# Kernel tuning notes

Measured on AMD Instinct MI355X. Metric: run time of the kernel, lower is better.

Reference implementation:

```python
import jax, jax.numpy as jnp
import numpy as np

# Mamba3/SSD selective state-space mixer (scalar-A-per-head SSD recurrence,
# causal depthwise conv on x/B/C, gated RMSNorm, in/out projections).
D_MODEL = 1024
EXPAND = 2
D_INNER = EXPAND * D_MODEL            # 2048
HEADDIM = D_MODEL // 16               # 64  (head_count=16 -> headdim 64)
NHEADS = D_INNER // HEADDIM           # 32
D_STATE = 128
CONV_W = 4
CONV_DIM = D_INNER + 2 * D_STATE      # x, B, C share the conv
D_IN_PROJ = 2 * D_INNER + 2 * D_STATE + NHEADS  # z, x, B, C, dt
EPS = 1e-5


def setup_inputs() -> dict:
    key = jax.random.key(0)
    ks = jax.random.split(key, 8)
    B, L = 4, 2048
    hidden = jax.random.normal(ks[0], (B, L, D_MODEL), dtype=jnp.float32)
    W_in = jax.random.normal(ks[1], (D_MODEL, D_IN_PROJ), dtype=jnp.float32) * 0.02
    conv_w = jax.random.normal(ks[2], (CONV_DIM, CONV_W), dtype=jnp.float32) * 0.2
    conv_b = jnp.zeros((CONV_DIM,), dtype=jnp.float32)
    # dt_bias: inverse-softplus of dt ~ U[1e-3, 0.1]
    dt = jnp.exp(jax.random.uniform(ks[3], (NHEADS,)) * (np.log(0.1) - np.log(1e-3)) + np.log(1e-3))
    dt_bias = dt + jnp.log(-jnp.expm1(-dt))
    A_log = jnp.log(jax.random.uniform(ks[4], (NHEADS,), minval=1.0, maxval=16.0))
    D = jnp.ones((NHEADS,), dtype=jnp.float32)
    norm_w = jnp.ones((D_INNER,), dtype=jnp.float32)
    W_out = jax.random.normal(ks[5], (D_INNER, D_MODEL), dtype=jnp.float32) * 0.02
    return {"hidden": hidden, "W_in": W_in, "conv_w": conv_w, "conv_b": conv_b,
            "dt_bias": dt_bias, "A_log": A_log, "D": D, "norm_w": norm_w, "W_out": W_out}


def _silu(x):
    return x * jax.nn.sigmoid(x)


def _mixer(hidden, W_in, conv_w, conv_b, dt_bias, A_log, D, norm_w, W_out):
    Bsz, L, _ = hidden.shape
    zxbcdt = hidden @ W_in                                    # [B,L,D_IN_PROJ]
    z = zxbcdt[..., :D_INNER]
    xBC = zxbcdt[..., D_INNER:D_INNER + CONV_DIM]
    dt = zxbcdt[..., -NHEADS:]                                # [B,L,H]
    # causal depthwise conv, width 4 (small fixed loop over taps)
    xp = jnp.pad(xBC, ((0, 0), (CONV_W - 1, 0), (0, 0)))
    conv = sum(xp[:, k:k + L, :] * conv_w[:, k] for k in range(CONV_W))
    xBC = _silu(conv + conv_b)
    x = xBC[..., :D_INNER].reshape(Bsz, L, NHEADS, HEADDIM)   # [B,L,H,P]
    Bm = xBC[..., D_INNER:D_INNER + D_STATE]                  # [B,L,N]
    Cm = xBC[..., D_INNER + D_STATE:]                         # [B,L,N]
    dt = jax.nn.softplus(dt + dt_bias)                        # [B,L,H]
    dA = jnp.exp(dt * (-jnp.exp(A_log)))                      # [B,L,H] decay in (0,1)
    dBx = jnp.einsum('blh,bln,blhp->blhpn', dt, Bm, x)        # [B,L,H,P,N]

    def step(h, inp):
        dA_t, dBx_t, C_t = inp                                # [B,H],[B,H,P,N],[B,N]
        h = dA_t[:, :, None, None] * h + dBx_t
        y = jnp.einsum('bhpn,bn->bhp', h, C_t)
        return h, y

    h0 = jnp.zeros((Bsz, NHEADS, HEADDIM, D_STATE), dtype=hidden.dtype)
    xs = (jnp.moveaxis(dA, 1, 0), jnp.moveaxis(dBx, 1, 0), jnp.moveaxis(Cm, 1, 0))
    _, ys = jax.lax.scan(step, h0, xs)                        # [L,B,H,P]
    y = jnp.moveaxis(ys, 0, 1) + D[None, None, :, None] * x   # skip term
    y = y.reshape(Bsz, L, D_INNER)
    # gated RMSNorm: norm(y * silu(z))
    y = y * _silu(z)
    y = y * jax.lax.rsqrt(jnp.mean(y * y, axis=-1, keepdims=True) + EPS) * norm_w
    return y @ W_out


def reference(hidden, W_in, conv_w, conv_b, dt_bias, A_log, D, norm_w, W_out):
    return _mixer(hidden, W_in, conv_w, conv_b, dt_bias, A_log, D, norm_w, W_out)
```

## Files before the change

kernel.cpp:

```cpp
#include <hip/hip_runtime.h>
#include <math.h>

#define BSZ 4
#define LEN 2048
#define DM 1024
#define DI 2048
#define HD 64
#define NH 32
#define DS 128
#define CD 2304
#define DP 4384
#define NTOK (BSZ*LEN)
#define QCH 128
#define NCH (LEN/QCH)
#define TOFF (DP-NH)

#define CONV_R 64
#define NRB (NTOK/CONV_R)
#define NPAD 4352

typedef unsigned short ushort_t;
typedef __bf16 bf16x8 __attribute__((ext_vector_type(8)));
typedef ushort_t us8 __attribute__((ext_vector_type(8)));
typedef float f32x4 __attribute__((ext_vector_type(4)));

__device__ __forceinline__ ushort_t f2bf(float f) {
    unsigned u = __float_as_uint(f);
    unsigned r = (u + 0x7FFFu + ((u >> 16) & 1u)) >> 16;
    return (ushort_t)r;
}
__device__ __forceinline__ float bf2f(ushort_t u) {
    return __uint_as_float(((unsigned)u) << 16);
}
__device__ __forceinline__ bf16x8 us2bf(us8 v) {
    union { us8 u; bf16x8 b; } x; x.u = v; return x.b;
}

__device__ __forceinline__ void gl_lds16(const void* g, void* l) {
    __builtin_amdgcn_global_load_lds(
        (const __attribute__((address_space(1))) void*)g,
        (__attribute__((address_space(3))) void*)l, 16, 0, 0);
}

__global__ __launch_bounds__(256) void cvt_bf16(
    const float* __restrict__ A, ushort_t* __restrict__ Ab)
{
    size_t i = ((size_t)blockIdx.x * 256 + threadIdx.x) * 4;
    float4 v = *(const float4*)(A + i);
    ushort_t o[4] = { f2bf(v.x), f2bf(v.y), f2bf(v.z), f2bf(v.w) };
    *(uint2*)(Ab + i) = *(uint2*)o;
}

__global__ __launch_bounds__(256) void transpose_cvt(
    const float* __restrict__ W, ushort_t* __restrict__ Wt,
    const float* __restrict__ colscale, int K, int N, int ldw)
{
    __shared__ float T[32][33];
    const int n0 = blockIdx.x * 32;
    const int k0 = blockIdx.y * 32;
    const int tid = threadIdx.x;
    #pragma unroll
    for (int l = 0; l < 4; l++) {
        int idx = tid + l * 256;
        int ki = idx >> 5, nj = idx & 31;
        int n = n0 + nj;
        float s = colscale ? colscale[k0 + ki] : 1.f;
        T[ki][nj] = (n < N) ? W[(size_t)(k0 + ki) * ldw + n] * s : 0.f;
    }
    __syncthreads();
    #pragma unroll
    for (int l = 0; l < 4; l++) {
        int idx = tid + l * 256;
        int nj = idx >> 5, ki = idx & 31;
        Wt[(size_t)(n0 + nj) * K + k0 + ki] = f2bf(T[ki][nj]);
    }
}

__global__ __launch_bounds__(256, 3) void gemm1_tb(
    const ushort_t* __restrict__ A, const ushort_t* __restrict__ Bt,
    ushort_t* __restrict__ C, int K, int lda, int ldb, int ldc)
{
    __shared__ __align__(16) ushort_t LA[3][128 * 32];
    __shared__ __align__(16) ushort_t LB[3][128 * 32];
    const int tid = threadIdx.x;
    int bid = blockIdx.y * gridDim.x + blockIdx.x;
    const int nwg = gridDim.x * gridDim.y;
    if (!(nwg & 7)) bid = (bid & 7) * (nwg >> 3) + (bid >> 3);
    const int n0 = (bid % gridDim.x) * 128;
    const int m0 = (bid / gridDim.x) * 128;
    const int lane = tid & 63;
    const int w = tid >> 6;
    const int wm = w >> 1, wn = w & 1;
    const int lm = lane & 15, quad = lane >> 4;
    const int ck = ((quad * 16) ^ (((lm >> 1) & 3) << 4)) >> 1;

    const int srow = tid >> 2;
    const int scolb = ((tid & 3) * 16) ^ (((tid >> 3) & 3) << 4);
    const char* gA = (const char*)A + ((size_t)(m0 + srow) * lda) * 2 + scolb;
    const char* gB = (const char*)Bt + ((size_t)(n0 + srow) * ldb) * 2 + scolb;
    const size_t strA = (size_t)64 * lda * 2;
    const size_t strB = (size_t)64 * ldb * 2;
    const int ldst = tid * 8;

    f32x4 acc[4][4];
    #pragma unroll
    for (int i = 0; i < 4; i++)
        #pragma unroll
        for (int j = 0; j < 4; j++) acc[i][j] = (f32x4){0.f, 0.f, 0.f, 0.f};

    const int NTt = K >> 5;

    auto STAGE = [&](int kt1, int buf) {
        const char* a = gA + (size_t)kt1 * 64;
        const char* b = gB + (size_t)kt1 * 64;
        gl_lds16(a + 0 * strA, &LA[buf][0 * 2048 + ldst]);
        gl_lds16(a + 1 * strA, &LA[buf][1 * 2048 + ldst]);
        gl_lds16(b + 0 * strB, &LB[buf][0 * 2048 + ldst]);
        gl_lds16(b + 1 * strB, &LB[buf][1 * 2048 + ldst]);
    };

    STAGE(0, 0);
    STAGE(1, 1);

    int cur = 0;
    int sb  = 2;
    for (int kt = 0; kt < NTt; ++kt) {
        __builtin_amdgcn_s_barrier();
        const int ahead = NTt - 1 - kt;
        if (ahead >= 2) {
            STAGE(kt + 2, sb);
            asm volatile("s_waitcnt vmcnt(8)" ::: "memory");
        } else if (ahead == 1) {
            asm volatile("s_waitcnt vmcnt(4)" ::: "memory");
        } else {
            asm volatile("s_waitcnt vmcnt(0)" ::: "memory");
        }
        __builtin_amdgcn_s_barrier();

        bf16x8 af[4], bf[4];
        #pragma unroll
        for (int s = 0; s < 4; s++)
            af[s] = *(const bf16x8*)&LA[cur][((wm * 64 + s * 16 + lm) << 5) + ck];
        #pragma unroll
        for (int t = 0; t < 4; t++)
            bf[t] = *(const bf16x8*)&LB[cur][((wn * 64 + t * 16 + lm) << 5) + ck];
        __builtin_amdgcn_s_setprio(1);
        #pragma unroll
        for (int s = 0; s < 4; s++)
            #pragma unroll
            for (int t = 0; t < 4; t++)
                acc[s][t] = __builtin_amdgcn_mfma_f32_16x16x32_bf16(
                    af[s], bf[t], acc[s][t], 0, 0, 0);
        __builtin_amdgcn_s_setprio(0);

        cur = (cur == 2) ? 0 : cur + 1;
        sb  = (sb == 2) ? 0 : sb + 1;
    }

    #pragma unroll
    for (int s = 0; s < 4; s++) {
        const int row = m0 + wm * 64 + s * 16 + quad * 4;
        #pragma unroll
        for (int t = 0; t < 4; t++) {
            const int col = n0 + wn * 64 + t * 16 + lm;
            #pragma unroll
            for (int r = 0; r < 4; r++)
                C[(size_t)(row + r) * ldc + col] = f2bf(acc[s][t][r]);
        }
    }
}

template <bool OB>
__global__ __launch_bounds__(256) void gemm128(
    const ushort_t* __restrict__ A, const ushort_t* __restrict__ Bt,
    void* __restrict__ Cp, const float* __restrict__ rowscale,
    int K, int lda, int ldb, int ldc)
{
    __shared__ __align__(16) ushort_t LA[2][128 * 64];
    __shared__ __align__(16) ushort_t LB[2][128 * 64];
    const int tid = threadIdx.x;
    int bid = blockIdx.y * gridDim.x + blockIdx.x;
    const int nwg = gridDim.x * gridDim.y;
    if (!(nwg & 7)) bid = (bid & 7) * (nwg >> 3) + (bid >> 3);
    const int n0 = (bid % gridDim.x) * 128;
    const int m0 = (bid / gridDim.x) * 128;
    const int lane = tid & 63;
    const int w = tid >> 6;
    const int wm = w >> 1, wn = w & 1;
    const int lm = lane & 15, quad = lane >> 4;
    const int swz = (lm & 7) << 4;
    const int ck0 = ((0 * 64 + quad * 16) ^ swz) >> 1;
    const int ck1 = ((1 * 64 + quad * 16) ^ swz) >> 1;

    const int srow = tid >> 3;
    const int scolb = ((tid & 7) * 16) ^ ((srow & 7) << 4);
    const char* gA = (const char*)A + ((size_t)(m0 + srow) * lda) * 2 + scolb;
    const char* gB = (const char*)Bt + ((size_t)(n0 + srow) * ldb) * 2 + scolb;
    const size_t strA = (size_t)32 * lda * 2;
    const size_t strB = (size_t)32 * ldb * 2;
    const int ldst = tid * 8;

    f32x4 acc[4][4];
    #pragma unroll
    for (int i = 0; i < 4; i++)
        #pragma unroll
        for (int j = 0; j < 4; j++) acc[i][j] = (f32x4){0.f, 0.f, 0.f, 0.f};

    const int NTt = K >> 6;

    auto STAGE = [&](int kt1, int nxt) {
        const char* a = gA + (size_t)kt1 * 128;
        const char* b = gB + (size_t)kt1 * 128;
        #pragma unroll
        for (int j = 0; j < 4; j++)
            gl_lds16(a + j * strA, &LA[nxt][j * 2048 + ldst]);
        #pragma unroll
        for (int j = 0; j < 4; j++)
            gl_lds16(b + j * strB, &LB[nxt][j * 2048 + ldst]);
    };

    STAGE(0, 0);

    for (int kt = 0; kt < NTt; ++kt) {
        const int cur = kt & 1;
        __builtin_amdgcn_s_barrier();
        if (kt + 1 < NTt) {
            STAGE(kt + 1, cur ^ 1);
            asm volatile("s_waitcnt vmcnt(8)" ::: "memory");
        } else {
            asm volatile("s_waitcnt vmcnt(0)" ::: "memory");
        }
        __builtin_amdgcn_s_barrier();

        bf16x8 af[4][2], bf[4][2];
        #pragma unroll
        for (int s = 0; s < 4; s++) {
            const int rb = (wm * 64 + s * 16 + lm) << 6;
            af[s][0] = *(const bf16x8*)&LA[cur][rb + ck0];
            af[s][1] = *(const bf16x8*)&LA[cur][rb + ck1];
        }
        #pragma unroll
        for (int t = 0; t < 4; t++) {
            const int rb = (wn * 64 + t * 16 + lm) << 6;
            bf[t][0] = *(const bf16x8*)&LB[cur][rb + ck0];
            bf[t][1] = *(const bf16x8*)&LB[cur][rb + ck1];
        }
        __builtin_amdgcn_s_setprio(1);
        #pragma unroll
        for (int kk = 0; kk < 2; kk++)
            #pragma unroll
            for (int s = 0; s < 4; s++)
                #pragma unroll
                for (int t = 0; t < 4; t++)
                    acc[s][t] = __builtin_amdgcn_mfma_f32_16x16x32_bf16(
                        af[s][kk], bf[t][kk], acc[s][t], 0, 0, 0);
        __builtin_amdgcn_s_setprio(0);
    }

    #pragma unroll
    for (int s = 0; s < 4; s++) {
        const int row = m0 + wm * 64 + s * 16 + quad * 4;
        float rs[4] = {1.f, 1.f, 1.f, 1.f};
        if (!OB && rowscale) {
            #pragma unroll
            for (int r = 0; r < 4; r++)
                rs[r] = rsqrtf(rowscale[row + r] * (1.f / DI) + 1e-5f);
        }
        #pragma unroll
        for (int t = 0; t < 4; t++) {
            const int col = n0 + wn * 64 + t * 16 + lm;
            #pragma unroll
            for (int r = 0; r < 4; r++) {
                if (OB)
                    ((ushort_t*)Cp)[(size_t)(row + r) * ldc + col] = f2bf(acc[s][t][r]);
                else
                    ((float*)Cp)[(size_t)(row + r) * ldc + col] = acc[s][t][r] * rs[r];
            }
        }
    }
}

__global__ __launch_bounds__(256) void conv_silu_bf16(
    const ushort_t* __restrict__ xbcb, const float* __restrict__ cw,
    const float* __restrict__ cb, ushort_t* __restrict__ xT,
    ushort_t* __restrict__ Bn, ushort_t* __restrict__ BT,
    ushort_t* __restrict__ Cn)
{
    __shared__ ushort_t Tl[256][68];
    const int tid = threadIdx.x;
    const int c = blockIdx.x * 256 + tid;
    const int rb = blockIdx.y;
    const int row0 = rb * CONV_R;
    const bool isBC = (blockIdx.x == 8);

    const float w0 = cw[c*4+0], w1 = cw[c*4+1], w2 = cw[c*4+2], w3 = cw[c*4+3];
    const float bias = cb[c];
    float h0 = 0.f, h1 = 0.f, h2 = 0.f;
    if ((row0 & (LEN - 1)) != 0) {
        h0 = bf2f(xbcb[(size_t)(row0 - 3) * NPAD + c]);
        h1 = bf2f(xbcb[(size_t)(row0 - 2) * NPAD + c]);
        h2 = bf2f(xbcb[(size_t)(row0 - 1) * NPAD + c]);
    }
    const ushort_t* p = xbcb + (size_t)row0 * NPAD + c;
    for (int r = 0; r < CONV_R; r++) {
        float xin = bf2f(*p);
        float a = bias + w0*h0 + w1*h1 + w2*h2 + w3*xin;
        ushort_t bv = f2bf(a / (1.f + __expf(-a)));
        Tl[tid][r] = bv;
        if (isBC) {
            int row = row0 + r;
            if (tid < DS) Bn[(size_t)row * DS + tid] = bv;
            else          Cn[(size_t)row * DS + (tid - DS)] = bv;
        }
        h0 = h1; h1 = h2; h2 = xin;
        p += NPAD;
    }
    __syncthreads();

    const int seg = tid & 7;
    const int clb = tid >> 3;
    if (!isBC) {
        #pragma unroll
        for (int pass = 0; pass < 8; pass++) {
            int cl = pass * 32 + clb;
            int cc = blockIdx.x * 256 + cl;
            us8 v;
            #pragma unroll
            for (int j = 0; j < 8; j++) v[j] = Tl[cl][seg * 8 + j];
            *(us8*)&xT[(size_t)cc * NTOK + row0 + seg * 8] = v;
        }
    } else {
        #pragma unroll
        for (int pass = 0; pass < 4; pass++) {
            int n = pass * 32 + clb;
            us8 v;
            #pragma unroll
            for (int j = 0; j < 8; j++) v[j] = Tl[n][seg * 8 + j];
            *(us8*)&BT[(size_t)n * NTOK + row0 + seg * 8] = v;
        }
    }
}

__global__ __launch_bounds__(256) void gct_gemm(
    const ushort_t* __restrict__ Bn, const ushort_t* __restrict__ Cn,
    float* __restrict__ Graw)
{
    const int bc = blockIdx.x;
    const int chunk = bc % NCH;
    const int b = bc / NCH;
    const size_t rowbase = (size_t)b * LEN + (size_t)chunk * QCH;
    const int tid = threadIdx.x;
    const int w = tid >> 6, lane = tid & 63;
    const int lm = lane & 15, quad = lane >> 4;
    const int tw0 = w * 32;

    f32x4 acc[2][8];
    #pragma unroll
    for (int ti = 0; ti < 2; ti++)
        #pragma unroll
        for (int sj = 0; sj < 8; sj++) acc[ti][sj] = (f32x4){0.f, 0.f, 0.f, 0.f};

    #pragma unroll
    for (int ks = 0; ks < 4; ks++) {
        const int k0 = ks * 32 + quad * 8;
        bf16x8 a0 = *(const bf16x8*)&Cn[(rowbase + tw0 + lm) * DS + k0];
        bf16x8 a1 = *(const bf16x8*)&Cn[(rowbase + tw0 + 16 + lm) * DS + k0];
        #pragma unroll
        for (int sj = 0; sj < 8; sj++) {
            bf16x8 bb = *(const bf16x8*)&Bn[(rowbase + sj * 16 + lm) * DS + k0];
            acc[0][sj] = __builtin_amdgcn_mfma_f32_16x16x32_bf16(a0, bb, acc[0][sj], 0, 0, 0);
            acc[1][sj] = __builtin_amdgcn_mfma_f32_16x16x32_bf16(a1, bb, acc[1][sj], 0, 0, 0);
        }
    }
    float* G = Graw + (size_t)bc * (QCH * QCH);
    #pragma unroll
    for (int ti = 0; ti < 2; ti++)
        #pragma unroll
        for (int sj = 0; sj < 8; sj++)
            #pragma unroll
            for (int r = 0; r < 4; r++)
                G[(size_t)(tw0 + ti * 16 + quad * 4 + r) * QCH + sj * 16 + lm] = acc[ti][sj][r];
}

__global__ __launch_bounds__(256) void dt_proc_fp32(
    const float* __restrict__ hidden, const float* __restrict__ W_in,
    const float* __restrict__ dt_bias, const float* __restrict__ A_log,
    float* __restrict__ dtv, float* __restrict__ ldA)
{
    const int h = threadIdx.x & 31;
    const int tt = threadIdx.x >> 5;
    const int t = blockIdx.x * 8 + tt;
    const float* hr = hidden + (size_t)t * DM;
    const float* wc = W_in + TOFF + h;
    float a0 = 0.f, a1 = 0.f, a2 = 0.f, a3 = 0.f;
    for (int k = 0; k < DM; k += 4) {
        a0 += hr[k+0] * wc[(size_t)(k+0) * DP];
        a1 += hr[k+1] * wc[(size_t)(k+1) * DP];
        a2 += hr[k+2] * wc[(size_t)(k+2) * DP];
        a3 += hr[k+3] * wc[(size_t)(k+3) * DP];
    }
    float v = (a0 + a1) + (a2 + a3) + dt_bias[h];
    float sp = (v > 20.f) ? v : log1pf(expf(v));
    int idx = t * NH + h;
    dtv[idx] = sp;
    ldA[idx] = -sp * expf(A_log[h]);
}

__global__ __launch_bounds__(64) void scan_chunk(
    const float* __restrict__ dtv, const float* __restrict__ ldA,
    float* __restrict__ lcpb, float* __restrict__ dtsb,
    float* __restrict__ coefb, float* __restrict__ csum)
{
    const int blk = blockIdx.x;
    const int chunk = blk % NCH;
    const int bh = blk / NCH;
    const int h = bh % NH;
    const int b = bh / NH;
    const int lane = threadIdx.x;
    const size_t rowbase = (size_t)b * LEN + (size_t)chunk * QCH;
    const int t0 = 2 * lane, t1 = 2 * lane + 1;
    float v0 = ldA[(rowbase + t0) * NH + h];
    float v1 = ldA[(rowbase + t1) * NH + h];
    float d0 = dtv[(rowbase + t0) * NH + h];
    float d1 = dtv[(rowbase + t1) * NH + h];
    float pair = v0 + v1;
    #pragma unroll
    for (int off = 1; off < 64; off <<= 1) {
        float n = __shfl_up(pair, off, 64);
        if (lane >= off) pair += n;
    }
    float l1 = pair, l0 = pair - v1;
    float total = __shfl(pair, 63, 64);
    size_t base = (size_t)blk * QCH;
    *(float2*)&lcpb[base + t0] = make_float2(l0, l1);
    *(float2*)&dtsb[base + t0] = make_float2(d0, d1);
    *(float2*)&coefb[base + t0] =
        make_float2(__expf(total - l0) * d0, __expf(total - l1) * d1);
    if (lane == 63) csum[blk] = total;
}

__global__ __launch_bounds__(256) void phase1_mfma(
    const ushort_t* __restrict__ xT, const ushort_t* __restrict__ BT,
    const float* __restrict__ coefb, float* __restrict__ S)
{
    const int h = blockIdx.x & (NH - 1);
    const int bc = blockIdx.x >> 5;
    const int chunk = bc % NCH;
    const int b = bc / NCH;
    const int blko = (b * NH + h) * NCH + chunk;
    const int tid = threadIdx.x;
    const size_t rowbase = (size_t)b * LEN + (size_t)chunk * QCH;

    __shared__ float coef[QCH];
    if (tid < QCH) coef[tid] = coefb[(size_t)blko * QCH + tid];
    __syncthreads();

    const int w = tid >> 6, lane = tid & 63;
    const int lm = lane & 15, quad = lane >> 4;
    const int nw0 = w * 32;

    f32x4 acc[4][2];
    #pragma unroll
    for (int i = 0; i < 4; i++)
        #pragma unroll
        for (int j = 0; j < 2; j++) acc[i][j] = (f32x4){0.f, 0.f, 0.f, 0.f};

    #pragma unroll
    for (int ks = 0; ks < 4; ks++) {
        const int k0 = ks * 32 + quad * 8;
        bf16x8 a[4];
        #pragma unroll
        for (int mi = 0; mi < 4; mi++)
            a[mi] = *(const bf16x8*)&xT[(size_t)(h * HD + mi * 16 + lm) * NTOK + rowbase + k0];
        float cf[8];
        #pragma unroll
        for (int j = 0; j < 8; j++) cf[j] = coef[k0 + j];
        #pragma unroll
        for (int ni = 0; ni < 2; ni++) {
            us8 raw = *(const us8*)&BT[(size_t)(nw0 + ni * 16 + lm) * NTOK + rowbase + k0];
            us8 sb;
            #pragma unroll
            for (int j = 0; j < 8; j++) sb[j] = f2bf(bf2f(raw[j]) * cf[j]);
            bf16x8 bfr = us2bf(sb);
            __builtin_amdgcn_s_setprio(1);
            #pragma unroll
            for (int mi = 0; mi < 4; mi++)
                acc[mi][ni] = __builtin_amdgcn_mfma_f32_16x16x32_bf16(a[mi], bfr, acc[mi][ni], 0, 0, 0);
            __builtin_amdgcn_s_setprio(0);
        }
    }
    float* Sb = S + (size_t)blko * (HD * DS);
    #pragma unroll
    for (int mi = 0; mi < 4; mi++)
        #pragma unroll
        for (int ni = 0; ni < 2; ni++)
            #pragma unroll
            for (int r = 0; r < 4; r++)
                Sb[(size_t)(mi * 16 + quad * 4 + r) * DS + nw0 + ni * 16 + lm] = acc[mi][ni][r];
}

__global__ __launch_bounds__(256) void phase2(
    const float* __restrict__ S, const float* __restrict__ csum,
    ushort_t* __restrict__ hsb)
{
    const int bh = blockIdx.x >> 3;
    const int esl = blockIdx.x & 7;
    const int tid = threadIdx.x;
    const int eb = esl * 1024 + tid;
    float run[4] = {0.f, 0.f, 0.f, 0.f};
    for (int c = 0; c < NCH; c++) {
        float P = __expf(csum[bh * NCH + c]);
        size_t base = (size_t)(bh * NCH + c) * (HD * DS);
        #pragma unroll
        for (int i = 0; i < 4; i++) {
            size_t idx = base + eb + i * 256;
            float s = S[idx];
            hsb[idx] = f2bf(run[i]);
            run[i] = P * run[i] + s;
        }
    }
}

__global__ __launch_bounds__(256) void phase3_mfma(
    const ushort_t* __restrict__ xT, const ushort_t* __restrict__ Cn,
    const ushort_t* __restrict__ hsb, const float* __restrict__ Graw,
    const float* __restrict__ lcpb, const float* __restrict__ dtsb,
    const float* __restrict__ Dvec, ushort_t* __restrict__ zxb,
    float* __restrict__ ss)
{
    const int tid = threadIdx.x;
    const int h = blockIdx.x & (NH - 1);
    const int bc = blockIdx.x >> 5;
    const int chunk = bc % NCH;
    const int b = bc / NCH;
    const int blko = (b * NH + h) * NCH + chunk;
    const size_t rowbase = (size_t)b * LEN + (size_t)chunk * QCH;

    __shared__ float lcp[QCH];
    __shared__ float dts[QCH];
    if (tid < QCH) {
        lcp[tid] = lcpb[(size_t)blko * QCH + tid];
        dts[tid] = dtsb[(size_t)blko * QCH + tid];
    }
    __syncthreads();

    const int w = tid >> 6, lane = tid & 63;
    const int lm = lane & 15, quad = lane >> 4;
    const int tw0 = w * 32;

    const float* Gr = Graw + (size_t)bc * (QCH * QCH);
    const ushort_t* hsp = hsb + (size_t)blko * (HD * DS);

    f32x4 acc2[2][4];
    #pragma unroll
    for (int ti = 0; ti < 2; ti++)
        #pragma unroll
        for (int pi = 0; pi < 4; pi++) acc2[ti][pi] = (f32x4){0.f, 0.f, 0.f, 0.f};

    #pragma unroll
    for (int ks = 0; ks < 8; ks++) {
        bf16x8 a[2], bb[4];
        if (ks < 4) {
            const int k0 = ks * 32 + quad * 8;
            #pragma unroll
            for (int ti = 0; ti < 2; ti++) {
                int t = tw0 + ti * 16 + lm;
                float lt = lcp[t];
                const float* gp = Gr + (size_t)t * QCH + k0;
                float4 g0 = *(const float4*)gp;
                float4 g1 = *(const float4*)(gp + 4);
                float ge[8] = { g0.x, g0.y, g0.z, g0.w, g1.x, g1.y, g1.z, g1.w };
                us8 sb;
                #pragma unroll
                for (int j = 0; j < 8; j++) {
                    int s = k0 + j;
                    float wv = (s <= t) ? (__expf(lt - lcp[s]) * dts[s]) : 0.f;
                    sb[j] = f2bf(ge[j] * wv);
                }
                a[ti] = us2bf(sb);
            }
            #pragma unroll
            for (int pi = 0; pi < 4; pi++)
                bb[pi] = *(const bf16x8*)&xT[(size_t)(h * HD + pi * 16 + lm) * NTOK + rowbase + k0];
        } else {
            const int k0 = (ks - 4) * 32 + quad * 8;
            #pragma unroll
            for (int ti = 0; ti < 2; ti++) {
                int t = tw0 + ti * 16 + lm;
                float sc = __expf(lcp[t]);
                us8 raw = *(const us8*)&Cn[(rowbase + t) * DS + k0];
                us8 sb;
                #pragma unroll
                for (int j = 0; j < 8; j++) sb[j] = f2bf(bf2f(raw[j]) * sc);
                a[ti] = us2bf(sb);
            }
            #pragma unroll
            for (int pi = 0; pi < 4; pi++)
                bb[pi] = *(const bf16x8*)&hsp[(size_t)(pi * 16 + lm) * DS + k0];
        }
        __builtin_amdgcn_s_setprio(1);
        #pragma unroll
        for (int ti = 0; ti < 2; ti++)
            #pragma unroll
            for (int pi = 0; pi < 4; pi++)
                acc2[ti][pi] = __builtin_amdgcn_mfma_f32_16x16x32_bf16(a[ti], bb[pi], acc2[ti][pi], 0, 0, 0);
        __builtin_amdgcn_s_setprio(0);
    }

    const float Dh = Dvec[h];
    float vsq[2][4] = {};
    #pragma unroll
    for (int ti = 0; ti < 2; ti++)
        #pragma unroll
        for (int pi = 0; pi < 4; pi++) {
            int tb = tw0 + ti * 16 + quad * 4;
            int col = h * HD + pi * 16 + lm;
            ushort4 xv = *(const ushort4*)&xT[(size_t)(h * HD + pi * 16 + lm) * NTOK + rowbase + tb];
            const ushort_t* xe = (const ushort_t*)&xv;
            #pragma unroll
            for (int r = 0; r < 4; r++) {
                size_t grow = rowbase + tb + r;
                float y = acc2[ti][pi][r] + Dh * bf2f(xe[r]);
                float z = bf2f(zxb[grow * NPAD + col]);
                float v = y * (z / (1.f + __expf(-z)));
                vsq[ti][r] += v * v;
                zxb[grow * NPAD + DI + col] = f2bf(v);
            }
        }
    #pragma unroll
    for (int ti = 0; ti < 2; ti++)
        #pragma unroll
        for (int r = 0; r < 4; r++) {
            float s = vsq[ti][r];
            s += __shfl_xor(s, 1, 64);
            s += __shfl_xor(s, 2, 64);
            s += __shfl_xor(s, 4, 64);
            s += __shfl_xor(s, 8, 64);
            if (lm == 0) {
                int tb = tw0 + ti * 16 + quad * 4 + r;
                atomicAdd(&ss[rowbase + tb], s);
            }
        }
}

extern "C" void kernel_launch(void* const* d_in, const int* in_sizes, int n_in,
                              void* d_out, int out_size, void* d_ws, size_t ws_size,
                              hipStream_t stream)
{
    const float* hidden  = (const float*)d_in[0];
    const float* W_in    = (const float*)d_in[1];
    const float* conv_w  = (const float*)d_in[2];
    const float* conv_b  = (const float*)d_in[3];
    const float* dt_bias = (const float*)d_in[4];
    const float* A_log   = (const float*)d_in[5];
    const float* Dv      = (const float*)d_in[6];
    const float* norm_w  = (const float*)d_in[7];
    const float* W_out   = (const float*)d_in[8];
    float* out = (float*)d_out;

    char* ws = (char*)d_ws;
    size_t o = 0;
    ushort_t* zxb  = (ushort_t*)(ws + o); o += (size_t)NTOK * NPAD * 2;
    float* S       = (float*)(ws + o);    o += (size_t)BSZ * NH * NCH * HD * DS * 4;
    ushort_t* xT   = (ushort_t*)(ws + o); o += (size_t)DI * NTOK * 2;
    ushort_t* Bn   = (ushort_t*)(ws + o); o += (size_t)NTOK * DS * 2;
    ushort_t* BT   = (ushort_t*)(ws + o); o += (size_t)DS * NTOK * 2;
    ushort_t* Cn   = (ushort_t*)(ws + o); o += (size_t)NTOK * DS * 2;
    ushort_t* hsb  = (ushort_t*)(ws + o); o += (size_t)BSZ * NH * NCH * HD * DS * 2;
    float* Graw    = (float*)(ws + o);    o += (size_t)BSZ * NCH * QCH * QCH * 4;
    float* dtv     = (float*)(ws + o);    o += (size_t)NTOK * NH * 4;
    float* ldA     = (float*)(ws + o);    o += (size_t)NTOK * NH * 4;
    float* lcpb    = (float*)(ws + o);    o += (size_t)BSZ * NH * LEN * 4;
    float* dtsb    = (float*)(ws + o);    o += (size_t)BSZ * NH * LEN * 4;
    float* coefb   = (float*)(ws + o);    o += (size_t)BSZ * NH * LEN * 4;
    float* csum    = (float*)(ws + o);    o += (size_t)BSZ * NH * NCH * 4;
    float* ss      = (float*)(ws + o);    o += (size_t)NTOK * 4;
    ushort_t* Ah   = (ushort_t*)S;
    ushort_t* W1t  = (ushort_t*)((char*)S + (size_t)NTOK * DM * 2);
    ushort_t* Wot  = hsb;
    ushort_t* xbcb = zxb + DI;
    ushort_t* ynb  = zxb + DI;

    hipMemsetAsync(ss, 0, (size_t)NTOK * 4, stream);
    cvt_bf16<<<(NTOK * DM) / 1024, 256, 0, stream>>>(hidden, Ah);
    transpose_cvt<<<dim3(NPAD / 32, DM / 32), 256, 0, stream>>>(
        W_in, W1t, nullptr, DM, NPAD, DP);
    gemm1_tb<<<dim3(NPAD / 128, NTOK / 128), 256, 0, stream>>>(
        Ah, W1t, zxb, DM, DM, DM, NPAD);
    conv_silu_bf16<<<dim3(CD / 256, NRB), 256, 0, stream>>>(
        xbcb, conv_w, conv_b, xT, Bn, BT, Cn);
    gct_gemm<<<BSZ * NCH, 256, 0, stream>>>(Bn, Cn, Graw);
    dt_proc_fp32<<<NTOK / 8, 256, 0, stream>>>(hidden, W_in, dt_bias, A_log, dtv, ldA);
    scan_chunk<<<BSZ * NH * NCH, 64, 0, stream>>>(dtv, ldA, lcpb, dtsb, coefb, csum);
    phase1_mfma<<<BSZ * NH * NCH, 256, 0, stream>>>(xT, BT, coefb, S);
    phase2<<<BSZ * NH * 8, 256, 0, stream>>>(S, csum, hsb);
    phase3_mfma<<<BSZ * NH * NCH, 256, 0, stream>>>(
        xT, Cn, hsb, Graw, lcpb, dtsb, Dv, zxb, ss);
    transpose_cvt<<<dim3(DM / 32, DI / 32), 256, 0, stream>>>(
        W_out, Wot, norm_w, DI, DM, DM);
    gemm128<false><<<dim3(DM / 128, NTOK / 128), 256, 0, stream>>>(
        ynb, Wot, out, ss, DI, NPAD, DI, DM);
}
```

Measured before the change: 498.1 us.

## Fuse chunk-state GEMM and inter-chunk scan into one sequential-per-head kernel

Merges phase1 (per-chunk state contributions via MFMA) and phase2 (inter-chunk recurrence) into one kernel. Each block owns one (batch, head, half of state dim) and loops over all chunks, keeping the running state in registers and writing only the bf16 prefix states. This removes the fp32 S buffer round trip and one launch. In exchange, the grid shrinks from 2048 blocks to 256, each processing 16 chunks serially, which lowers parallelism and latency hiding.

```diff
diff --git a/kernel.cpp b/kernel.cpp
--- a/kernel.cpp
+++ b/kernel.cpp
@@ -439,45 +439,45 @@
     if (lane == 63) csum[blk] = total;
 }
 
-__global__ __launch_bounds__(256) void phase1_mfma(
+__global__ __launch_bounds__(256) void phase12_fused(
     const ushort_t* __restrict__ xT, const ushort_t* __restrict__ BT,
-    const float* __restrict__ coefb, float* __restrict__ S)
-{
-    const int h = blockIdx.x & (NH - 1);
-    const int bc = blockIdx.x >> 5;
-    const int chunk = bc % NCH;
-    const int b = bc / NCH;
-    const int blko = (b * NH + h) * NCH + chunk;
+    const float* __restrict__ coefb, const float* __restrict__ csum,
+    ushort_t* __restrict__ hsb)
+{
+    const int blk = blockIdx.x;
+    const int nhalf = blk & 1;
+    const int bh = blk >> 1;
+    const int h = bh & (NH - 1);
+    const int b = bh >> 5;
     const int tid = threadIdx.x;
-    const size_t rowbase = (size_t)b * LEN + (size_t)chunk * QCH;
-
-    __shared__ float coef[QCH];
-    if (tid < QCH) coef[tid] = coefb[(size_t)blko * QCH + tid];
-    __syncthreads();
-
     const int w = tid >> 6, lane = tid & 63;
     const int lm = lane & 15, quad = lane >> 4;
-    const int nw0 = w * 32;
-
-    f32x4 acc[4][2];
-    #pragma unroll
-    for (int i = 0; i < 4; i++)
-        #pragma unroll
-        for (int j = 0; j < 2; j++) acc[i][j] = (f32x4){0.f, 0.f, 0.f, 0.f};
-
-    #pragma unroll
-    for (int ks = 0; ks < 4; ks++) {
-        const int k0 = ks * 32 + quad * 8;
-        bf16x8 a[4];
-        #pragma unroll
-        for (int mi = 0; mi < 4; mi++)
-            a[mi] = *(const bf16x8*)&xT[(size_t)(h * HD + mi * 16 + lm) * NTOK + rowbase + k0];
-        float cf[8];
-        #pragma unroll
-        for (int j = 0; j < 8; j++) cf[j] = coef[k0 + j];
-        #pragma unroll
-        for (int ni = 0; ni < 2; ni++) {
-            us8 raw = *(const us8*)&BT[(size_t)(nw0 + ni * 16 + lm) * NTOK + rowbase + k0];
+    const int nw0 = nhalf * 64 + w * 16;
+
+    f32x4 run[4];
+    #pragma unroll
+    for (int mi = 0; mi < 4; mi++) run[mi] = (f32x4){0.f, 0.f, 0.f, 0.f};
+
+    for (int c = 0; c < NCH; c++) {
+        const size_t rowbase = (size_t)b * LEN + (size_t)c * QCH;
+        const size_t cb = ((size_t)bh * NCH + c) * QCH;
+        const float P = __expf(csum[bh * NCH + c]);
+
+        f32x4 acc[4];
+        #pragma unroll
+        for (int mi = 0; mi < 4; mi++) acc[mi] = (f32x4){0.f, 0.f, 0.f, 0.f};
+
+        #pragma unroll
+        for (int ks = 0; ks < 4; ks++) {
+            const int k0 = ks * 32 + quad * 8;
+            bf16x8 a[4];
+            #pragma unroll
+            for (int mi = 0; mi < 4; mi++)
+                a[mi] = *(const bf16x8*)&xT[(size_t)(h * HD + mi * 16 + lm) * NTOK + rowbase + k0];
+            float4 c0 = *(const float4*)&coefb[cb + k0];
+            float4 c1 = *(const float4*)&coefb[cb + k0 + 4];
+            float cf[8] = { c0.x, c0.y, c0.z, c0.w, c1.x, c1.y, c1.z, c1.w };
+            us8 raw = *(const us8*)&BT[(size_t)(nw0 + lm) * NTOK + rowbase + k0];
             us8 sb;
             #pragma unroll
             for (int j = 0; j < 8; j++) sb[j] = f2bf(bf2f(raw[j]) * cf[j]);
@@ -485,39 +485,21 @@
             __builtin_amdgcn_s_setprio(1);
             #pragma unroll
             for (int mi = 0; mi < 4; mi++)
-                acc[mi][ni] = __builtin_amdgcn_mfma_f32_16x16x32_bf16(a[mi], bfr, acc[mi][ni], 0, 0, 0);
+                acc[mi] = __builtin_amdgcn_mfma_f32_16x16x32_bf16(a[mi], bfr, acc[mi], 0, 0, 0);
             __builtin_amdgcn_s_setprio(0);
         }
-    }
-    float* Sb = S + (size_t)blko * (HD * DS);
-    #pragma unroll
-    for (int mi = 0; mi < 4; mi++)
-        #pragma unroll
-        for (int ni = 0; ni < 2; ni++)
+
+        ushort_t* hb = hsb + ((size_t)bh * NCH + c) * (HD * DS);
+        #pragma unroll
+        for (int mi = 0; mi < 4; mi++)
             #pragma unroll
             for (int r = 0; r < 4; r++)
-                Sb[(size_t)(mi * 16 + quad * 4 + r) * DS + nw0 + ni * 16 + lm] = acc[mi][ni][r];
-}
-
-__global__ __launch_bounds__(256) void phase2(
-    const float* __restrict__ S, const float* __restrict__ csum,
-    ushort_t* __restrict__ hsb)
-{
-    const int bh = blockIdx.x >> 3;
-    const int esl = blockIdx.x & 7;
-    const int tid = threadIdx.x;
-    const int eb = esl * 1024 + tid;
-    float run[4] = {0.f, 0.f, 0.f, 0.f};
-    for (int c = 0; c < NCH; c++) {
-        float P = __expf(csum[bh * NCH + c]);
-        size_t base = (size_t)(bh * NCH + c) * (HD * DS);
-        #pragma unroll
-        for (int i = 0; i < 4; i++) {
-            size_t idx = base + eb + i * 256;
-            float s = S[idx];
-            hsb[idx] = f2bf(run[i]);
-            run[i] = P * run[i] + s;
-        }
+                hb[(size_t)(mi * 16 + quad * 4 + r) * DS + nw0 + lm] = f2bf(run[mi][r]);
+        #pragma unroll
+        for (int mi = 0; mi < 4; mi++)
+            #pragma unroll
+            for (int r = 0; r < 4; r++)
+                run[mi][r] = P * run[mi][r] + acc[mi][r];
     }
 }
 
@@ -675,6 +657,7 @@
     float* coefb   = (float*)(ws + o);    o += (size_t)BSZ * NH * LEN * 4;
     float* csum    = (float*)(ws + o);    o += (size_t)BSZ * NH * NCH * 4;
     float* ss      = (float*)(ws + o);    o += (size_t)NTOK * 4;
+    (void)S;
     ushort_t* Ah   = (ushort_t*)S;
     ushort_t* W1t  = (ushort_t*)((char*)S + (size_t)NTOK * DM * 2);
     ushort_t* Wot  = hsb;
@@ -692,8 +675,7 @@
     gct_gemm<<<BSZ * NCH, 256, 0, stream>>>(Bn, Cn, Graw);
     dt_proc_fp32<<<NTOK / 8, 256, 0, stream>>>(hidden, W_in, dt_bias, A_log, dtv, ldA);
     scan_chunk<<<BSZ * NH * NCH, 64, 0, stream>>>(dtv, ldA, lcpb, dtsb, coefb, csum);
-    phase1_mfma<<<BSZ * NH * NCH, 256, 0, stream>>>(xT, BT, coefb, S);
-    phase2<<<BSZ * NH * 8, 256, 0, stream>>>(S, csum, hsb);
+    phase12_fused<<<BSZ * NH * 2, 256, 0, stream>>>(xT, BT, coefb, csum, hsb);
     phase3_mfma<<<BSZ * NH * NCH, 256, 0, stream>>>(
         xT, Cn, hsb, Graw, lcpb, dtsb, Dv, zxb, ss);
     transpose_cvt<<<dim3(DM / 32, DI / 32), 256, 0, stream>>>(
```

After: 496.7 us. Within noise of the previous version (-0.3%).
